# Kernel optimization log

Hardware: AMD Instinct MI355X
Metric: run time of the kernel (lower is better)

## Reference

```python
import jax, jax.numpy as jnp
import numpy as np

EPS = 1e-5
GROUPS = 8


def conv3x3(x, w, b):
    # x: [B,Cin,H,W], w: [Cout,Cin,3,3]
    y = jax.lax.conv_general_dilated(x, w, (1, 1), 'SAME',
                                     dimension_numbers=('NCHW', 'OIHW', 'NCHW'))
    return y + b[None, :, None, None]


def group_norm(x, scale, bias):
    B, C, H, W = x.shape
    xg = x.reshape(B, GROUPS, C // GROUPS, H, W)
    mu = jnp.mean(xg, axis=(2, 3, 4), keepdims=True)
    var = jnp.var(xg, axis=(2, 3, 4), keepdims=True)
    xn = ((xg - mu) * jax.lax.rsqrt(var + EPS)).reshape(B, C, H, W)
    return xn * scale[None, :, None, None] + bias[None, :, None, None]


def setup_inputs() -> dict:
    key = jax.random.key(0)
    ks = jax.random.split(key, 18)
    B, C, D, H, W = 8, 256, 128, 128, 128
    s = 0.02
    return {
        'current_feat': jax.random.normal(ks[0], (B, C, H, W), jnp.float32),
        'prev_hidden': jax.random.normal(ks[1], (B, D, H, W), jnp.float32),
        'conv1_w': jax.random.normal(ks[2], (D, C, 3, 3), jnp.float32) * s,
        'conv1_b': jnp.zeros((D,), jnp.float32),
        'gn_scale': jnp.ones((D,), jnp.float32),
        'gn_bias': jnp.zeros((D,), jnp.float32),
        'ce_w1': jax.random.normal(ks[3], (64, 4), jnp.float32) * 0.5,
        'ce_b1': jnp.zeros((64,), jnp.float32),
        'ce_w2': jax.random.normal(ks[4], (D, 64), jnp.float32) * 0.125,
        'ce_b2': jnp.zeros((D,), jnp.float32),
        'w_ih': jax.random.normal(ks[5], (3 * D, 3 * D), jnp.float32) * s,
        'b_ih': jnp.zeros((3 * D,), jnp.float32),
        'w_hh': jax.random.normal(ks[6], (3 * D, D), jnp.float32) * s,
        'b_hh': jnp.zeros((3 * D,), jnp.float32),
        'conv2_w': jax.random.normal(ks[7], (C, D, 3, 3), jnp.float32) * s,
        'conv2_b': jnp.zeros((C,), jnp.float32),
    }


def reference(current_feat, prev_hidden, conv1_w, conv1_b, gn_scale, gn_bias,
              ce_w1, ce_b1, ce_w2, ce_b2, w_ih, b_ih, w_hh, b_hh,
              conv2_w, conv2_b):
    B, C, H, W = current_feat.shape
    D = conv1_w.shape[0]

    # spatial_proj: conv -> GroupNorm(8) -> exact GELU
    spatial = jax.nn.gelu(group_norm(conv3x3(current_feat, conv1_w, conv1_b),
                                     gn_scale, gn_bias), approximate=False)

    # coordinate embedding (Linear(4,64) -> ReLU -> Linear(64,D))
    xc = jnp.broadcast_to(jnp.linspace(-1.0, 1.0, W)[None, None, :], (B, H, W))
    yc = jnp.broadcast_to(jnp.linspace(-1.0, 1.0, H)[None, :, None], (B, H, W))
    coord = jnp.stack([xc, yc, xc * H, yc * W], axis=-1)       # [B,H,W,4]
    ce = jax.nn.relu(coord @ ce_w1.T + ce_b1) @ ce_w2.T + ce_b2  # [B,H,W,D]
    coord_emb = jnp.transpose(ce, (0, 3, 1, 2))                 # [B,D,H,W]

    # batched GRUCell over all B*H*W positions (no spatial recurrence)
    gru_in = jnp.concatenate([spatial, coord_emb, prev_hidden], axis=1)  # [B,3D,H,W]
    Xf = jnp.transpose(gru_in, (0, 2, 3, 1)).reshape(-1, 3 * D)          # [N,3D]
    hf = jnp.transpose(prev_hidden, (0, 2, 3, 1)).reshape(-1, D)         # [N,D]
    gi = Xf @ w_ih.T + b_ih
    gh = hf @ w_hh.T + b_hh
    i_r, i_z, i_n = jnp.split(gi, 3, axis=-1)
    h_r, h_z, h_n = jnp.split(gh, 3, axis=-1)
    r = jax.nn.sigmoid(i_r + h_r)
    z = jax.nn.sigmoid(i_z + h_z)
    n = jnp.tanh(i_n + r * h_n)
    h_new = (1.0 - z) * n + z * hf                                       # [N,D]
    new_hidden = jnp.transpose(h_new.reshape(B, H, W, D), (0, 3, 1, 2))  # [B,D,H,W]

    # output_proj (Dropout2d inactive in eval) + residual
    output_feat = conv3x3(new_hidden, conv2_w, conv2_b) + current_feat
    return output_feat, new_hidden
```

## Files before the change

kernel.cpp:

```cpp
#include <hip/hip_runtime.h>
#include <math.h>

#define BH 8
#define HH 128
#define WW 128
#define HW 16384

typedef __attribute__((ext_vector_type(8))) short bf16x8;
typedef __attribute__((ext_vector_type(4))) float f32x4;

__device__ inline unsigned short f2bf(float f) {
    union { float f; unsigned u; } v; v.f = f;
    unsigned r = v.u + 0x7FFF + ((v.u >> 16) & 1);
    return (unsigned short)(r >> 16);
}
__device__ inline float bf2f(unsigned short u) {
    union { unsigned u; float f; } v; v.u = (unsigned)u << 16;
    return v.f;
}

typedef const __attribute__((address_space(1))) void* gptr_t;
typedef __attribute__((address_space(3))) void* lptr_t;
__device__ inline void gload_lds16(const void* g, void* l) {
    __builtin_amdgcn_global_load_lds((gptr_t)g, (lptr_t)l, 16, 0, 0);
}

__global__ __launch_bounds__(256) void transpose_cast(
        const float* __restrict__ in, unsigned short* __restrict__ out, int C) {
    __shared__ float T[32][65];
    int tid = threadIdx.x;
    int pb = blockIdx.x * 64, cb = blockIdx.y * 32, b = blockIdx.z;
    #pragma unroll
    for (int j = 0; j < 8; ++j) {
        int idx = tid + j * 256;
        int c = idx >> 6, p = idx & 63;
        T[c][p] = in[((size_t)(b * C + cb + c)) * HW + pb + p];
    }
    __syncthreads();
    #pragma unroll
    for (int j = 0; j < 8; ++j) {
        int idx = tid + j * 256;
        int p = idx >> 5, c = idx & 31;
        out[((size_t)(b * HW + pb + p)) * C + cb + c] = f2bf(T[c][p]);
    }
}

__global__ __launch_bounds__(256) void repack_weights(
        const float* __restrict__ w1, const float* __restrict__ w2,
        const float* __restrict__ wih, const float* __restrict__ whh,
        unsigned short* __restrict__ w1t, unsigned short* __restrict__ w2t,
        unsigned short* __restrict__ wg) {
    int i = blockIdx.x * 256 + threadIdx.x;
    if (i < 294912) {
        int t = i >> 15, rem = i & 32767, d = rem >> 8, c = rem & 255;
        w1t[i] = f2bf(w1[((size_t)(d * 256 + c)) * 9 + t]);
    }
    if (i < 294912) {
        int t = i >> 15, co = (i >> 7) & 255, ci = i & 127;
        w2t[i] = f2bf(w2[((size_t)(co * 128 + ci)) * 9 + t]);
    }
    if (i < 196608) {
        int m = i / 384, k = i - m * 384;
        float v = 0.0f;
        if (m < 384) {
            if (k < 128)       v = wih[(size_t)m * 384 + k];
            else if (k < 256)  v = wih[(size_t)m * 384 + 256 + (k - 128)];
            else               v = (m < 256) ? whh[(size_t)m * 128 + (k - 256)] : 0.0f;
        } else {
            v = (k >= 256) ? whh[(size_t)(m - 128) * 128 + (k - 256)] : 0.0f;
        }
        wg[i] = f2bf(v);
    }
}

__global__ __launch_bounds__(256) void prep_ce(
        const float* __restrict__ w2, const float* __restrict__ b2,
        const float* __restrict__ wih,
        float* __restrict__ M, float* __restrict__ cebias) {
    int i = blockIdx.x * 256 + threadIdx.x;
    if (i < 24576) {
        int j = i / 384, m = i - j * 384;
        float acc = 0.0f;
        for (int d = 0; d < 128; ++d)
            acc = fmaf(w2[(size_t)d * 64 + j], wih[(size_t)m * 384 + 128 + d], acc);
        M[i] = acc;
    } else if (i < 24960) {
        int m = i - 24576;
        float acc = 0.0f;
        for (int d = 0; d < 128; ++d)
            acc = fmaf(b2[d], wih[(size_t)m * 384 + 128 + d], acc);
        cebias[m] = acc;
    }
}

__global__ __launch_bounds__(384) void ce_g_kernel(
        const float* __restrict__ w1, const float* __restrict__ b1,
        const float* __restrict__ M, const float* __restrict__ cebias,
        float* __restrict__ ce_g) {
    __shared__ float h1[16][64];
    int m = threadIdx.x;
    int pos0 = blockIdx.x * 16;
    for (int e = m; e < 1024; e += 384) {
        int p = e >> 6, j = e & 63;
        int pos = pos0 + p;
        int hh = pos >> 7, wp = pos & 127;
        float xc = -1.0f + 2.0f * (float)wp / 127.0f;
        float yc = -1.0f + 2.0f * (float)hh / 127.0f;
        float a = xc * w1[j*4+0] + yc * w1[j*4+1]
                + xc * 128.0f * w1[j*4+2] + yc * 128.0f * w1[j*4+3] + b1[j];
        h1[p][j] = fmaxf(a, 0.0f);
    }
    __syncthreads();
    float acc[16];
    float cb = cebias[m];
    #pragma unroll
    for (int p = 0; p < 16; ++p) acc[p] = cb;
    for (int j = 0; j < 64; ++j) {
        float Mv = M[(size_t)j * 384 + m];
        #pragma unroll
        for (int p = 0; p < 16; ++p)
            acc[p] = fmaf(h1[p][j], Mv, acc[p]);
    }
    #pragma unroll
    for (int p = 0; p < 16; ++p)
        ce_g[(size_t)(pos0 + p) * 384 + m] = acc[p];
}

template<int CIN, int COUT, bool CONV1>
__global__ __launch_bounds__(256, 2) void conv_mfma(
        const unsigned short* __restrict__ xt,
        const unsigned short* __restrict__ wt,
        const float* __restrict__ bias,
        float* __restrict__ stats_acc,
        const float* __restrict__ resid,
        unsigned short* __restrict__ y_bf,
        float* __restrict__ y_f32,
        const unsigned short* __restrict__ zbuf) {
    constexpr int NCC = CIN / 32;
    constexpr int NT  = 3 * NCC;
    __shared__ unsigned short Ash[2][130 * 32];
    __shared__ unsigned short Wsh[2][384 * 32];

    const int tid = threadIdx.x;
    const int h = blockIdx.x, b = blockIdx.y;
    const int cobase = blockIdx.z * 128;
    const int lane = tid & 63, wave = tid >> 6;
    const int wn = (wave & 1) * 64, wd = (wave >> 1) * 64;
    const int l15 = lane & 15, quad = lane >> 4;

    f32x4 acc[4][4];
    #pragma unroll
    for (int i = 0; i < 4; ++i)
        #pragma unroll
        for (int j = 0; j < 4; ++j)
            acc[i][j] = (f32x4){0.f, 0.f, 0.f, 0.f};

    auto stage = [&](int buf, int t) {
        const int kh = t / NCC, cc = t - kh * NCC;
        const int r = h + kh - 1;
        const bool oob = ((unsigned)r >= (unsigned)HH);
        const char* abase = oob ? (const char*)zbuf
            : (const char*)(xt + ((size_t)(b * HW + r * WW)) * CIN + cc * 32);
        #pragma unroll
        for (int j = 0; j < 2; ++j) {
            const int ob = 64 + (tid + j * 256) * 16;
            const int row = ob >> 6, cb = ob & 63;
            const int sel = (row >> 1) & 3;
            const char* src = oob ? abase + cb
                : abase + (size_t)(row - 1) * (CIN * 2) + (cb ^ (sel << 4));
            gload_lds16(src, (char*)Ash[buf] + 64 + (wave * 64 + j * 256) * 16);
        }
        #pragma unroll
        for (int j = 0; j < 6; ++j) {
            const int ob = (tid + j * 256) * 16;
            const int m = ob >> 6, cb = ob & 63;
            const int sel = (m >> 1) & 3;
            const int kw = m >> 7, d = m & 127;
            const char* src = (const char*)wt
                + (((size_t)(kh * 3 + kw) * COUT + cobase + d) * CIN + cc * 32) * 2
                + (cb ^ (sel << 4));
            gload_lds16(src, (char*)Wsh[buf] + (wave * 64 + j * 256) * 16);
        }
    };

    if (tid < 16) {
        int buf = tid >> 3, hi = (tid >> 2) & 1, q = tid & 3;
        *(f32x4*)((char*)Ash[buf] + (hi ? 129 * 64 : 0) + q * 16) =
            (f32x4){0.f, 0.f, 0.f, 0.f};
    }
    stage(0, 0);
    __syncthreads();

    int curb = 0;
    for (int t = 0; t < NT; ++t) {
        if (t + 1 < NT) stage(curb ^ 1, t + 1);
        #pragma unroll
        for (int kw = 0; kw < 3; ++kw) {
            bf16x8 a[4], bb[4];
            #pragma unroll
            for (int fn = 0; fn < 4; ++fn) {
                int ra = wn + fn * 16 + l15 + kw;
                a[fn] = *(const bf16x8*)&Ash[curb][ra * 32 +
                            (quad * 8 ^ (((ra >> 1) & 3) << 3))];
            }
            #pragma unroll
            for (int fd = 0; fd < 4; ++fd) {
                int m = kw * 128 + wd + fd * 16 + l15;
                bb[fd] = *(const bf16x8*)&Wsh[curb][m * 32 +
                            (quad * 8 ^ (((m >> 1) & 3) << 3))];
            }
            #pragma unroll
            for (int fn = 0; fn < 4; ++fn)
                #pragma unroll
                for (int fd = 0; fd < 4; ++fd)
                    acc[fn][fd] = __builtin_amdgcn_mfma_f32_16x16x32_bf16(
                        a[fn], bb[fd], acc[fn][fd], 0, 0, 0);
        }
        __syncthreads();
        curb ^= 1;
    }

    if (CONV1) {
        float gsum[4] = {0.f,0.f,0.f,0.f}, gss[4] = {0.f,0.f,0.f,0.f};
        #pragma unroll
        for (int fd = 0; fd < 4; ++fd) {
            int d = wd + fd * 16 + l15;
            float bv = bias[d];
            #pragma unroll
            for (int fn = 0; fn < 4; ++fn) {
                #pragma unroll
                for (int reg = 0; reg < 4; ++reg) {
                    int n = wn + fn * 16 + quad * 4 + reg;
                    float v = acc[fn][fd][reg] + bv;
                    y_bf[((size_t)(b * HW + h * WW + n)) * 128 + d] = f2bf(v);
                    gsum[fd] += v; gss[fd] += v * v;
                }
            }
        }
        #pragma unroll
        for (int fd = 0; fd < 4; ++fd) {
            float s = gsum[fd], q = gss[fd];
            for (int o = 32; o > 0; o >>= 1) {
                s += __shfl_down(s, o);
                q += __shfl_down(q, o);
            }
            if (lane == 0) {
                int g = (wd >> 4) + fd;
                atomicAdd(&stats_acc[(b * 8 + g) * 2], s);
                atomicAdd(&stats_acc[(b * 8 + g) * 2 + 1], q);
            }
        }
    } else {
        #pragma unroll
        for (int fd = 0; fd < 4; ++fd) {
            int co = cobase + wd + fd * 16 + l15;
            float bv = bias[co];
            #pragma unroll
            for (int fn = 0; fn < 4; ++fn) {
                int n0 = wn + fn * 16 + quad * 4;
                size_t ofs = ((size_t)(b * 256 + co)) * HW + h * WW + n0;
                float4 rs = *(const float4*)(resid + ofs);
                float4 o;
                o.x = acc[fn][fd][0] + bv + rs.x;
                o.y = acc[fn][fd][1] + bv + rs.y;
                o.z = acc[fn][fd][2] + bv + rs.z;
                o.w = acc[fn][fd][3] + bv + rs.w;
                *(float4*)(y_f32 + ofs) = o;
            }
        }
    }
}

__global__ void gn_finalize(float* stats) {
    int t = threadIdx.x;
    if (t < 64) {
        float s = stats[t*2], q = stats[t*2+1];
        const float inv = 1.0f / 262144.0f;
        float mean = s * inv;
        float var = q * inv - mean * mean;
        stats[t*2] = mean;
        stats[t*2+1] = rsqrtf(var + 1e-5f);
    }
}

__global__ __launch_bounds__(256) void gn_gelu(
        unsigned short* __restrict__ y, const float* __restrict__ stats,
        const float* __restrict__ scale, const float* __restrict__ bias) {
    size_t i = (size_t)blockIdx.x * 256 + threadIdx.x;
    size_t e = i * 4;
    int d = (int)(e & 127);
    int b = (int)(e >> 21);
    int g = b * 8 + (d >> 4);
    float mean = stats[g * 2], rstd = stats[g * 2 + 1];
    ushort4 v = *(ushort4*)&y[e];
    unsigned short vs[4] = {v.x, v.y, v.z, v.w};
    #pragma unroll
    for (int j = 0; j < 4; ++j) {
        float a = rstd * scale[d + j];
        float c = bias[d + j] - mean * a;
        float t = bf2f(vs[j]) * a + c;
        vs[j] = f2bf(0.5f * t * (1.0f + erff(t * 0.70710678118654752f)));
    }
    ushort4 o = {vs[0], vs[1], vs[2], vs[3]};
    *(ushort4*)&y[e] = o;
}

__global__ __launch_bounds__(256, 2) void gru_gemm(
        const unsigned short* __restrict__ sp_t,
        const unsigned short* __restrict__ ph_t,
        const unsigned short* __restrict__ wg,
        unsigned short* __restrict__ G) {
    __shared__ unsigned short Xs[2][128 * 32];
    __shared__ unsigned short Wgs[2][128 * 32];
    const int tid = threadIdx.x;
    const int nt = blockIdx.x, mt = blockIdx.y;
    const size_t p0 = (size_t)nt * 128;
    const int lane = tid & 63, wave = tid >> 6;
    const int wn = (wave & 1) * 64, wm = (wave >> 1) * 64;
    const int l15 = lane & 15, quad = lane >> 4;

    f32x4 acc[4][4];
    #pragma unroll
    for (int i = 0; i < 4; ++i)
        #pragma unroll
        for (int j = 0; j < 4; ++j)
            acc[i][j] = (f32x4){0.f, 0.f, 0.f, 0.f};

    auto stage = [&](int buf, int ck) {
        const int k0 = ck * 32;
        const char* xb = (const char*)((k0 < 128)
            ? sp_t + p0 * 128 + k0
            : ph_t + p0 * 128 + (k0 & 127));
        #pragma unroll
        for (int j = 0; j < 2; ++j) {
            const int ob = (tid + j * 256) * 16;
            const int row = ob >> 6, cb = ob & 63;
            const int sel = (row >> 1) & 3;
            gload_lds16(xb + (size_t)row * 256 + (cb ^ (sel << 4)),
                        (char*)Xs[buf] + (wave * 64 + j * 256) * 16);
        }
        #pragma unroll
        for (int j = 0; j < 2; ++j) {
            const int ob = (tid + j * 256) * 16;
            const int row = ob >> 6, cb = ob & 63;
            const int sel = (row >> 1) & 3;
            gload_lds16((const char*)wg +
                            ((size_t)(mt * 128 + row) * 384 + k0) * 2 +
                            (cb ^ (sel << 4)),
                        (char*)Wgs[buf] + (wave * 64 + j * 256) * 16);
        }
    };

    stage(0, 0);
    __syncthreads();
    int curb = 0;
    for (int ck = 0; ck < 12; ++ck) {
        if (ck + 1 < 12) stage(curb ^ 1, ck + 1);
        bf16x8 a[4], bb[4];
        #pragma unroll
        for (int fn = 0; fn < 4; ++fn) {
            int row = wn + fn * 16 + l15;
            a[fn] = *(const bf16x8*)&Xs[curb][row * 32 +
                        (quad * 8 ^ (((row >> 1) & 3) << 3))];
        }
        #pragma unroll
        for (int fm = 0; fm < 4; ++fm) {
            int row = wm + fm * 16 + l15;
            bb[fm] = *(const bf16x8*)&Wgs[curb][row * 32 +
                        (quad * 8 ^ (((row >> 1) & 3) << 3))];
        }
        #pragma unroll
        for (int fn = 0; fn < 4; ++fn)
            #pragma unroll
            for (int fm = 0; fm < 4; ++fm)
                acc[fn][fm] = __builtin_amdgcn_mfma_f32_16x16x32_bf16(
                    a[fn], bb[fm], acc[fn][fm], 0, 0, 0);
        __syncthreads();
        curb ^= 1;
    }
    #pragma unroll
    for (int fm = 0; fm < 4; ++fm) {
        int m = mt * 128 + wm + fm * 16 + l15;
        #pragma unroll
        for (int fn = 0; fn < 4; ++fn)
            #pragma unroll
            for (int reg = 0; reg < 4; ++reg) {
                int n = wn + fn * 16 + quad * 4 + reg;
                G[(p0 + n) * 512 + m] = f2bf(acc[fn][fm][reg]);
            }
    }
}

__global__ __launch_bounds__(256) void gru_gate(
        const unsigned short* __restrict__ G,
        const float* __restrict__ ce_g,
        const float* __restrict__ b_ih, const float* __restrict__ b_hh,
        const float* __restrict__ prev_f32,
        float* __restrict__ new_hidden, unsigned short* __restrict__ hn_t) {
    __shared__ float T[128][65];
    const int tid = threadIdx.x;
    const size_t p0 = (size_t)blockIdx.x * 64;
    const int b = (int)(p0 >> 14);
    const int hw0 = (int)(p0 & (HW - 1));
    const int d = tid & 127;
    const float br  = b_ih[d]       + b_hh[d];
    const float bz  = b_ih[128 + d] + b_hh[128 + d];
    const float bin = b_ih[256 + d];
    const float bhn = b_hh[256 + d];
    for (int j = 0; j < 32; ++j) {
        int pp = (tid >> 7) + j * 2;
        size_t gbase = (p0 + pp) * 512;
        size_t cbase = (size_t)(hw0 + pp) * 384;
        float rl = bf2f(G[gbase + d])       + ce_g[cbase + d]       + br;
        float zl = bf2f(G[gbase + 128 + d]) + ce_g[cbase + 128 + d] + bz;
        float il = bf2f(G[gbase + 256 + d]) + ce_g[cbase + 256 + d] + bin;
        float hl = bf2f(G[gbase + 384 + d]) + bhn;
        float r = 1.0f / (1.0f + expf(-rl));
        float z = 1.0f / (1.0f + expf(-zl));
        float n = tanhf(il + r * hl);
        float hp = prev_f32[((size_t)(b * 128 + d)) * HW + hw0 + pp];
        float hn = (1.0f - z) * n + z * hp;
        T[d][pp] = hn;
        hn_t[(p0 + pp) * 128 + d] = f2bf(hn);
    }
    __syncthreads();
    #pragma unroll
    for (int j = 0; j < 8; ++j) {
        int idx = tid + j * 256;
        int d2 = idx >> 4, pp4 = (idx & 15) * 4;
        float4 v = { T[d2][pp4], T[d2][pp4+1], T[d2][pp4+2], T[d2][pp4+3] };
        *(float4*)&new_hidden[((size_t)(b * 128 + d2)) * HW + hw0 + pp4] = v;
    }
}

extern "C" void kernel_launch(void* const* d_in, const int* in_sizes, int n_in,
                              void* d_out, int out_size, void* d_ws, size_t ws_size,
                              hipStream_t stream) {
    const float* current_feat = (const float*)d_in[0];
    const float* prev_hidden  = (const float*)d_in[1];
    const float* conv1_w = (const float*)d_in[2];
    const float* conv1_b = (const float*)d_in[3];
    const float* gn_scale = (const float*)d_in[4];
    const float* gn_bias  = (const float*)d_in[5];
    const float* ce_w1 = (const float*)d_in[6];
    const float* ce_b1 = (const float*)d_in[7];
    const float* ce_w2 = (const float*)d_in[8];
    const float* ce_b2 = (const float*)d_in[9];
    const float* w_ih = (const float*)d_in[10];
    const float* b_ih = (const float*)d_in[11];
    const float* w_hh = (const float*)d_in[12];
    const float* b_hh = (const float*)d_in[13];
    const float* conv2_w = (const float*)d_in[14];
    const float* conv2_b = (const float*)d_in[15];

    char* ws = (char*)d_ws;
    unsigned short* cf_t = (unsigned short*)(ws);
    unsigned short* ph_t = (unsigned short*)(ws + 67108864);
    unsigned short* sp_t = (unsigned short*)(ws + 100663296);
    unsigned short* w1t  = (unsigned short*)(ws + 134217728);
    unsigned short* w2t  = (unsigned short*)(ws + 134807552);
    unsigned short* wg   = (unsigned short*)(ws + 135397376);
    float* Mmat          = (float*)(ws + 135790592);
    float* cebias        = (float*)(ws + 135888896);
    float* stats         = (float*)(ws + 135890432);
    unsigned short* zbuf = (unsigned short*)(ws + 135890944);
    unsigned short* hn_t = cf_t;
    float* ce_g          = (float*)(ws + 33554432);
    unsigned short* G    = (unsigned short*)d_out;
    float* out_feat      = (float*)d_out;
    float* new_hidden    = (float*)d_out + 33554432;

    hipMemsetAsync(stats, 0, 512, stream);
    hipMemsetAsync(zbuf, 0, 256, stream);
    hipLaunchKernelGGL(repack_weights, dim3(1152), dim3(256), 0, stream,
                       conv1_w, conv2_w, w_ih, w_hh, w1t, w2t, wg);
    hipLaunchKernelGGL(prep_ce, dim3(98), dim3(256), 0, stream,
                       ce_w2, ce_b2, w_ih, Mmat, cebias);
    hipLaunchKernelGGL(transpose_cast, dim3(256, 8, 8), dim3(256), 0, stream,
                       current_feat, cf_t, 256);
    hipLaunchKernelGGL(transpose_cast, dim3(256, 4, 8), dim3(256), 0, stream,
                       prev_hidden, ph_t, 128);
    hipLaunchKernelGGL((conv_mfma<256, 128, true>), dim3(128, 8, 1), dim3(256), 0, stream,
                       cf_t, w1t, conv1_b, stats, nullptr, sp_t, nullptr, zbuf);
    hipLaunchKernelGGL(ce_g_kernel, dim3(1024), dim3(384), 0, stream,
                       ce_w1, ce_b1, Mmat, cebias, ce_g);
    hipLaunchKernelGGL(gn_finalize, dim3(1), dim3(64), 0, stream, stats);
    hipLaunchKernelGGL(gn_gelu, dim3(16384), dim3(256), 0, stream,
                       sp_t, stats, gn_scale, gn_bias);
    hipLaunchKernelGGL(gru_gemm, dim3(1024, 4), dim3(256), 0, stream,
                       sp_t, ph_t, wg, G);
    hipLaunchKernelGGL(gru_gate, dim3(2048), dim3(256), 0, stream,
                       G, ce_g, b_ih, b_hh, prev_hidden, new_hidden, hn_t);
    hipLaunchKernelGGL((conv_mfma<128, 256, false>), dim3(128, 8, 2), dim3(256), 0, stream,
                       hn_t, w2t, conv2_b, nullptr, current_feat, nullptr, out_feat, zbuf);
}
```

Before: 1.039 ms.

## Load conv and GRU weight fragments directly into registers, drop weight LDS staging

In both the conv and GRU GEMM kernels, the weight tiles are no longer staged through double-buffered shared memory. Each lane now loads its MFMA B-fragments straight from global memory (L2-resident weights) into registers at the start of every k-step. Launch bounds rise to 3 and 4 waves per SIMD, since the smaller LDS footprint allows more resident blocks. The risk is that these global loads are not prefetched ahead and are issued right before the MFMAs, which can expose L2 latency, while cutting occupancy headroom for registers may also cause spills.

```diff
diff --git a/kernel.cpp b/kernel.cpp
--- a/kernel.cpp
+++ b/kernel.cpp
@@ -127,7 +127,7 @@
 }
 
 template<int CIN, int COUT, bool CONV1>
-__global__ __launch_bounds__(256, 2) void conv_mfma(
+__global__ __launch_bounds__(256, 3) void conv_mfma(
         const unsigned short* __restrict__ xt,
         const unsigned short* __restrict__ wt,
         const float* __restrict__ bias,
@@ -139,7 +139,6 @@
     constexpr int NCC = CIN / 32;
     constexpr int NT  = 3 * NCC;
     __shared__ unsigned short Ash[2][130 * 32];
-    __shared__ unsigned short Wsh[2][384 * 32];
 
     const int tid = threadIdx.x;
     const int h = blockIdx.x, b = blockIdx.y;
@@ -155,7 +154,9 @@
         for (int j = 0; j < 4; ++j)
             acc[i][j] = (f32x4){0.f, 0.f, 0.f, 0.f};
 
-    auto stage = [&](int buf, int t) {
+    const unsigned short* wlane = wt + (size_t)(cobase + wd + l15) * CIN + quad * 8;
+
+    auto stageA = [&](int buf, int t) {
         const int kh = t / NCC, cc = t - kh * NCC;
         const int r = h + kh - 1;
         const bool oob = ((unsigned)r >= (unsigned)HH);
@@ -170,17 +171,6 @@
                 : abase + (size_t)(row - 1) * (CIN * 2) + (cb ^ (sel << 4));
             gload_lds16(src, (char*)Ash[buf] + 64 + (wave * 64 + j * 256) * 16);
         }
-        #pragma unroll
-        for (int j = 0; j < 6; ++j) {
-            const int ob = (tid + j * 256) * 16;
-            const int m = ob >> 6, cb = ob & 63;
-            const int sel = (m >> 1) & 3;
-            const int kw = m >> 7, d = m & 127;
-            const char* src = (const char*)wt
-                + (((size_t)(kh * 3 + kw) * COUT + cobase + d) * CIN + cc * 32) * 2
-                + (cb ^ (sel << 4));
-            gload_lds16(src, (char*)Wsh[buf] + (wave * 64 + j * 256) * 16);
-        }
     };
 
     if (tid < 16) {
@@ -188,15 +178,23 @@
         *(f32x4*)((char*)Ash[buf] + (hi ? 129 * 64 : 0) + q * 16) =
             (f32x4){0.f, 0.f, 0.f, 0.f};
     }
-    stage(0, 0);
+    stageA(0, 0);
     __syncthreads();
 
     int curb = 0;
     for (int t = 0; t < NT; ++t) {
-        if (t + 1 < NT) stage(curb ^ 1, t + 1);
+        const int kh = t / NCC, cc = t - kh * NCC;
+        bf16x8 wreg[3][4];
+        #pragma unroll
+        for (int kw = 0; kw < 3; ++kw)
+            #pragma unroll
+            for (int fd = 0; fd < 4; ++fd)
+                wreg[kw][fd] = *(const bf16x8*)(wlane
+                    + (size_t)((kh * 3 + kw) * COUT + fd * 16) * CIN + cc * 32);
+        if (t + 1 < NT) stageA(curb ^ 1, t + 1);
         #pragma unroll
         for (int kw = 0; kw < 3; ++kw) {
-            bf16x8 a[4], bb[4];
+            bf16x8 a[4];
             #pragma unroll
             for (int fn = 0; fn < 4; ++fn) {
                 int ra = wn + fn * 16 + l15 + kw;
@@ -204,17 +202,11 @@
                             (quad * 8 ^ (((ra >> 1) & 3) << 3))];
             }
             #pragma unroll
-            for (int fd = 0; fd < 4; ++fd) {
-                int m = kw * 128 + wd + fd * 16 + l15;
-                bb[fd] = *(const bf16x8*)&Wsh[curb][m * 32 +
-                            (quad * 8 ^ (((m >> 1) & 3) << 3))];
-            }
-            #pragma unroll
             for (int fn = 0; fn < 4; ++fn)
                 #pragma unroll
                 for (int fd = 0; fd < 4; ++fd)
                     acc[fn][fd] = __builtin_amdgcn_mfma_f32_16x16x32_bf16(
-                        a[fn], bb[fd], acc[fn][fd], 0, 0, 0);
+                        a[fn], wreg[kw][fd], acc[fn][fd], 0, 0, 0);
         }
         __syncthreads();
         curb ^= 1;
@@ -305,13 +297,12 @@
     *(ushort4*)&y[e] = o;
 }
 
-__global__ __launch_bounds__(256, 2) void gru_gemm(
+__global__ __launch_bounds__(256, 4) void gru_gemm(
         const unsigned short* __restrict__ sp_t,
         const unsigned short* __restrict__ ph_t,
         const unsigned short* __restrict__ wg,
         unsigned short* __restrict__ G) {
     __shared__ unsigned short Xs[2][128 * 32];
-    __shared__ unsigned short Wgs[2][128 * 32];
     const int tid = threadIdx.x;
     const int nt = blockIdx.x, mt = blockIdx.y;
     const size_t p0 = (size_t)nt * 128;
@@ -326,7 +317,9 @@
         for (int j = 0; j < 4; ++j)
             acc[i][j] = (f32x4){0.f, 0.f, 0.f, 0.f};
 
-    auto stage = [&](int buf, int ck) {
+    const unsigned short* wlane = wg + (size_t)(mt * 128 + wm + l15) * 384 + quad * 8;
+
+    auto stageX = [&](int buf, int ck) {
         const int k0 = ck * 32;
         const char* xb = (const char*)((k0 < 128)
             ? sp_t + p0 * 128 + k0
@@ -339,24 +332,19 @@
             gload_lds16(xb + (size_t)row * 256 + (cb ^ (sel << 4)),
                         (char*)Xs[buf] + (wave * 64 + j * 256) * 16);
         }
-        #pragma unroll
-        for (int j = 0; j < 2; ++j) {
-            const int ob = (tid + j * 256) * 16;
-            const int row = ob >> 6, cb = ob & 63;
-            const int sel = (row >> 1) & 3;
-            gload_lds16((const char*)wg +
-                            ((size_t)(mt * 128 + row) * 384 + k0) * 2 +
-                            (cb ^ (sel << 4)),
-                        (char*)Wgs[buf] + (wave * 64 + j * 256) * 16);
-        }
     };
 
-    stage(0, 0);
+    stageX(0, 0);
     __syncthreads();
     int curb = 0;
     for (int ck = 0; ck < 12; ++ck) {
-        if (ck + 1 < 12) stage(curb ^ 1, ck + 1);
-        bf16x8 a[4], bb[4];
+        const int k0 = ck * 32;
+        bf16x8 wreg[4];
+        #pragma unroll
+        for (int fm = 0; fm < 4; ++fm)
+            wreg[fm] = *(const bf16x8*)(wlane + (size_t)(fm * 16) * 384 + k0);
+        if (ck + 1 < 12) stageX(curb ^ 1, ck + 1);
+        bf16x8 a[4];
         #pragma unroll
         for (int fn = 0; fn < 4; ++fn) {
             int row = wn + fn * 16 + l15;
@@ -364,17 +352,11 @@
                         (quad * 8 ^ (((row >> 1) & 3) << 3))];
         }
         #pragma unroll
-        for (int fm = 0; fm < 4; ++fm) {
-            int row = wm + fm * 16 + l15;
-            bb[fm] = *(const bf16x8*)&Wgs[curb][row * 32 +
-                        (quad * 8 ^ (((row >> 1) & 3) << 3))];
-        }
-        #pragma unroll
         for (int fn = 0; fn < 4; ++fn)
             #pragma unroll
             for (int fm = 0; fm < 4; ++fm)
                 acc[fn][fm] = __builtin_amdgcn_mfma_f32_16x16x32_bf16(
-                    a[fn], bb[fm], acc[fn][fm], 0, 0, 0);
+                    a[fn], wreg[fm], acc[fn][fm], 0, 0, 0);
         __syncthreads();
         curb ^= 1;
     }
```

New measurement: 1.219 ms. 17.3% more time.
